# Performance work log

Hardware: AMD Instinct MI355X
Metric: run time of the kernel (lower is better)

The kernel has to match this reference:

```python
import jax, jax.numpy as jnp
import numpy as np

LN_EPS = 1e-5


def _gather(x, idx):
    # x: [B, N, C], idx: [B, N, K] -> [B, N, K, C]
    return jax.vmap(lambda xb, ib: xb[ib])(x, idx)


def setup_inputs() -> dict:
    key = jax.random.key(0)
    ks = jax.random.split(key, 8)
    B, N, K, C_in, C_out, GEO = 2, 16384, 32, 128, 128, 10
    return {
        "points": jax.random.normal(ks[0], (B, N, 3), dtype=jnp.float32),
        "features": jax.random.normal(ks[1], (B, N, C_in), dtype=jnp.float32),
        "grouped_idx": jax.random.randint(ks[2], (B, N, K), 0, N, dtype=jnp.int32),
        "w_pos": jax.random.normal(ks[3], (GEO, C_in), dtype=jnp.float32) * (GEO ** -0.5),
        "b_pos": jnp.zeros((C_in,), jnp.float32),
        "w_gcm": jax.random.normal(ks[4], (C_in, C_in), dtype=jnp.float32) * (C_in ** -0.5),
        "b_gcm": jnp.zeros((C_in,), jnp.float32),
        "w_out": jax.random.normal(ks[5], (C_in, C_out), dtype=jnp.float32) * (C_in ** -0.5),
        "b_out": jnp.zeros((C_out,), jnp.float32),
        "ln_g": jnp.ones((C_out,), jnp.float32),
        "ln_b": jnp.zeros((C_out,), jnp.float32),
    }


def reference(points, features, grouped_idx, w_pos, b_pos, w_gcm, b_gcm,
              w_out, b_out, ln_g, ln_b):
    # gather neighbor coords and features: [B, N, K, *]
    grouped_pts = _gather(points, grouped_idx)
    xyz = points[..., 0:3]                      # [B, N, 3]
    grouped_xyz = grouped_pts[..., 0:3]         # [B, N, K, 3]
    center = xyz[:, :, None, :]                 # [B, N, 1, 3]
    diff = grouped_xyz - center                 # xi - xj
    dist = jnp.linalg.norm(diff, axis=-1, keepdims=True)  # ||xi - xj||
    K = grouped_xyz.shape[2]
    geo = jnp.concatenate(
        [jnp.broadcast_to(center, grouped_xyz.shape), grouped_xyz, diff, dist],
        axis=-1)                                # [B, N, K, 10]
    expanded_f = geo @ w_pos + b_pos            # pos_proj -> [B, N, K, C_in]
    grouped_f = _gather(features, grouped_idx)  # [B, N, K, C_in]
    h = jax.nn.relu((grouped_f + expanded_f) @ w_gcm + b_gcm)  # gcm_layer
    pooled = jnp.max(h, axis=2)                 # maxpooling over neighbors
    res = pooled + features                     # residual
    o = res @ w_out + b_out                     # out Linear
    mu = jnp.mean(o, axis=-1, keepdims=True)
    var = jnp.mean((o - mu) ** 2, axis=-1, keepdims=True)
    o = (o - mu) * jax.lax.rsqrt(var + LN_EPS) * ln_g + ln_b  # LayerNorm
    return jax.nn.relu(o)
```

## Files before the change

kernel.cpp:

```cpp
#include <hip/hip_runtime.h>
#include <hip/hip_bf16.h>
#include <math.h>

typedef __attribute__((ext_vector_type(8))) short short8;
typedef __attribute__((ext_vector_type(4))) float float4v;
typedef unsigned short ushort_t;

constexpr int NPTS = 32768;
constexpr int NN   = 16384;
constexpr int KK   = 32;
constexpr int CC   = 128;
constexpr int GRP  = 16;
constexpr int SR   = 132;
#define LN_EPS 1e-5f

constexpr size_t WS_PG = 0;
constexpr size_t WS_BE = 5120;
constexpr size_t WS_WP = 8192;
constexpr size_t WS_WO = 40960;
constexpr size_t WS_FW = 73728;

__device__ __forceinline__ short f2bs(float x) {
    return (short)__builtin_bit_cast(unsigned short, __float2bfloat16(x));
}
__device__ __forceinline__ float bs2f(ushort_t u) {
    return __uint_as_float(((unsigned)u) << 16);
}

__global__ __launch_bounds__(128) void prep_fold(
    const float* __restrict__ w_pos, const float* __restrict__ b_pos,
    const float* __restrict__ w_gcm, const float* __restrict__ b_gcm,
    const float* __restrict__ w_out,
    float* __restrict__ wsPG, float* __restrict__ wsBeff,
    short* __restrict__ wsWp, short* __restrict__ wsWo)
{
    const int c = threadIdx.x, g = blockIdx.x;
    if (g < 10) {
        float s = 0.f;
        #pragma unroll
        for (int r = 0; r < 128; ++r) s += w_pos[g * 128 + r] * w_gcm[r * 128 + c];
        wsPG[g * 128 + c] = s;
        return;
    }
    if (g == 10) {
        float s = b_gcm[c];
        #pragma unroll
        for (int r = 0; r < 128; ++r) s += b_pos[r] * w_gcm[r * 128 + c];
        wsBeff[c] = s;
        return;
    }
    if (g == 11) {
        #pragma unroll 4
        for (int e = c; e < 16 * 128 * 8; e += 128) {
            const int j = e & 7, n = (e >> 3) & 127, kg = e >> 10;
            wsWp[e] = f2bs(w_gcm[(kg * 8 + j) * 128 + n]);
        }
        return;
    }
    #pragma unroll 4
    for (int e = c; e < 16 * 128 * 8; e += 128) {
        const int j = e & 7, n = (e >> 3) & 127, kg = e >> 10;
        wsWo[e] = f2bs(w_out[(kg * 8 + j) * 128 + n]);
    }
}

__global__ __launch_bounds__(256) void fw_gemm(
    const float* __restrict__ F, const short* __restrict__ wsWp,
    ushort_t* __restrict__ fwbf)
{
    const int t = threadIdx.x, wv = t >> 6;
    const int quad = (t >> 4) & 3, m = t & 15;
    const int rg = wv >> 1, ch = wv & 1;
    const int r0 = blockIdx.x * 32 + rg * 16;

    short8 bW[4][4];
    #pragma unroll
    for (int ks = 0; ks < 4; ++ks)
        #pragma unroll
        for (int n = 0; n < 4; ++n)
            bW[ks][n] = ((const short8*)wsWp)[(ks * 4 + quad) * 128 + ch * 64 + n * 16 + m];

    const float* fr = F + (size_t)(r0 + m) * CC;
    short8 A[4];
    #pragma unroll
    for (int ks = 0; ks < 4; ++ks) {
        const float4 x = *(const float4*)(fr + ks * 32 + quad * 8);
        const float4 y = *(const float4*)(fr + ks * 32 + quad * 8 + 4);
        short8 v;
        v[0]=f2bs(x.x); v[1]=f2bs(x.y); v[2]=f2bs(x.z); v[3]=f2bs(x.w);
        v[4]=f2bs(y.x); v[5]=f2bs(y.y); v[6]=f2bs(y.z); v[7]=f2bs(y.w);
        A[ks] = v;
    }

    float4v acc[4] = {};
    #pragma unroll
    for (int ks = 0; ks < 4; ++ks)
        #pragma unroll
        for (int n = 0; n < 4; ++n)
            acc[n] = __builtin_amdgcn_mfma_f32_16x16x32_bf16(A[ks], bW[ks][n], acc[n], 0, 0, 0);

    #pragma unroll
    for (int n = 0; n < 4; ++n)
        #pragma unroll
        for (int r = 0; r < 4; ++r)
            fwbf[(size_t)(r0 + quad * 4 + r) * CC + ch * 64 + n * 16 + m] =
                (ushort_t)(unsigned short)f2bs(acc[n][r]);
}

__global__ __launch_bounds__(256) void bridge_gather(
    const float* __restrict__ points, const float* __restrict__ features,
    const int*   __restrict__ gidx,
    const float* __restrict__ wsPG, const float* __restrict__ wsBeff,
    const ushort_t* __restrict__ fwbf, const short* __restrict__ wsWo,
    const float* __restrict__ b_out, const float* __restrict__ ln_g,
    const float* __restrict__ ln_b,
    float* __restrict__ out)
{
    __shared__ float4 sND[GRP * KK];
    __shared__ int    sOff[GRP * KK];
    __shared__ float4 sCen[GRP];
    __shared__ short  sRes[GRP * SR];

    float* sPS = (float*)&sND[0];
    float* sPQ = sPS + 4 * GRP;

    const int t = threadIdx.x, wv = t >> 6;
    const int quad = (t >> 4) & 3, m = t & 15;
    const int sub = t >> 7, c = t & 127;
    const int g0 = blockIdx.x * GRP;
    const int nbase = (g0 >= NN) ? NN : 0;

    #pragma unroll
    for (int e = t; e < GRP * KK; e += 256) {
        const int p = e >> 5;
        const int kn = gidx[(size_t)(g0 + p) * KK + (e & 31)];
        const int row = nbase + kn;
        const float nx = points[(size_t)row * 3 + 0];
        const float ny = points[(size_t)row * 3 + 1];
        const float nz = points[(size_t)row * 3 + 2];
        const float cx = points[(size_t)(g0 + p) * 3 + 0];
        const float cy = points[(size_t)(g0 + p) * 3 + 1];
        const float cz = points[(size_t)(g0 + p) * 3 + 2];
        const float dx = nx - cx, dy = ny - cy, dz = nz - cz;
        sND[e] = make_float4(nx, ny, nz, sqrtf(dx * dx + dy * dy + dz * dz));
        sOff[e] = row << 8;
    }
    if (t < GRP) {
        sCen[t] = make_float4(points[(size_t)(g0 + t) * 3 + 0],
                              points[(size_t)(g0 + t) * 3 + 1],
                              points[(size_t)(g0 + t) * 3 + 2], 0.f);
    }

    float pg[10];
    #pragma unroll
    for (int g = 0; g < 10; ++g) pg[g] = wsPG[g * 128 + c];
    const float pga0 = pg[0] - pg[6], pga1 = pg[1] - pg[7], pga2 = pg[2] - pg[8];
    const float pgb0 = pg[3] + pg[6], pgb1 = pg[4] + pg[7], pgb2 = pg[5] + pg[8];
    const float pgd  = pg[9];
    const float be   = wsBeff[c];

    __syncthreads();

    const char* fwc = (const char*)fwbf + c * 2;
    for (int i = 0; i < GRP / 2; ++i) {
        const int p = sub * (GRP / 2) + i;
        const float4* nd = sND + p * KK;
        const int*    of = sOff + p * KK;
        float acc = -INFINITY;
        #pragma unroll 8
        for (int k = 0; k < KK; ++k) {
            const float4 g = nd[k];
            const float fw = bs2f(*(const ushort_t*)(fwc + of[k]));
            float v = fw + g.w * pgd;
            v = fmaf(g.x, pgb0, v);
            v = fmaf(g.y, pgb1, v);
            v = fmaf(g.z, pgb2, v);
            acc = fmaxf(acc, v);
        }
        const float4 cen = sCen[p];
        const float base = fmaf(cen.x, pga0, fmaf(cen.y, pga1, fmaf(cen.z, pga2, be)));
        const float pooled = fmaxf(acc + base, 0.f);
        const float res = pooled + features[(size_t)(g0 + p) * CC + c];
        sRes[p * SR + c] = f2bs(res);
    }
    __syncthreads();

    const int col0 = wv * 32 + m;
    short8 bWo[4][2];
    #pragma unroll
    for (int ks = 0; ks < 4; ++ks)
        #pragma unroll
        for (int ntl = 0; ntl < 2; ++ntl)
            bWo[ks][ntl] = ((const short8*)wsWo)[(ks * 4 + quad) * 128 + col0 + ntl * 16];

    const short* rm = sRes + m * SR;
    float4v acc2[2] = {};
    #pragma unroll
    for (int ks = 0; ks < 4; ++ks) {
        const short8 a = *(const short8*)(rm + ks * 32 + quad * 8);
        acc2[0] = __builtin_amdgcn_mfma_f32_16x16x32_bf16(a, bWo[ks][0], acc2[0], 0, 0, 0);
        acc2[1] = __builtin_amdgcn_mfma_f32_16x16x32_bf16(a, bWo[ks][1], acc2[1], 0, 0, 0);
    }

    const float boutv[2] = { b_out[col0], b_out[col0 + 16] };
    const float lngv[2]  = { ln_g[col0], ln_g[col0 + 16] };
    const float lnbv[2]  = { ln_b[col0], ln_b[col0 + 16] };

    #pragma unroll
    for (int r = 0; r < 4; ++r) {
        const float o0 = acc2[0][r] + boutv[0];
        const float o1 = acc2[1][r] + boutv[1];
        float ss = o0 + o1, qq = o0 * o0 + o1 * o1;
        #pragma unroll
        for (int d = 1; d < 16; d <<= 1) { ss += __shfl_xor(ss, d); qq += __shfl_xor(qq, d); }
        if (m == 0) { sPS[wv * GRP + quad * 4 + r] = ss; sPQ[wv * GRP + quad * 4 + r] = qq; }
    }
    __syncthreads();

    #pragma unroll
    for (int r = 0; r < 4; ++r) {
        const int R = quad * 4 + r;
        const float S = sPS[0 * GRP + R] + sPS[1 * GRP + R] + sPS[2 * GRP + R] + sPS[3 * GRP + R];
        const float Q = sPQ[0 * GRP + R] + sPQ[1 * GRP + R] + sPQ[2 * GRP + R] + sPQ[3 * GRP + R];
        const float mu  = S * (1.f / 128.f);
        const float var = fmaxf(Q * (1.f / 128.f) - mu * mu, 0.f);
        const float rstd = rsqrtf(var + LN_EPS);
        const float o0 = acc2[0][r] + boutv[0];
        const float o1 = acc2[1][r] + boutv[1];
        const size_t base = (size_t)(g0 + R) * CC;
        out[base + col0]      = fmaxf((o0 - mu) * rstd * lngv[0] + lnbv[0], 0.f);
        out[base + col0 + 16] = fmaxf((o1 - mu) * rstd * lngv[1] + lnbv[1], 0.f);
    }
}

extern "C" void kernel_launch(void* const* d_in, const int* in_sizes, int n_in,
                              void* d_out, int out_size, void* d_ws, size_t ws_size,
                              hipStream_t stream) {
    const float* points   = (const float*)d_in[0];
    const float* features = (const float*)d_in[1];
    const int*   gidx     = (const int*)  d_in[2];
    const float* w_pos    = (const float*)d_in[3];
    const float* b_pos    = (const float*)d_in[4];
    const float* w_gcm    = (const float*)d_in[5];
    const float* b_gcm    = (const float*)d_in[6];
    const float* w_out    = (const float*)d_in[7];
    const float* b_out    = (const float*)d_in[8];
    const float* ln_g     = (const float*)d_in[9];
    const float* ln_b     = (const float*)d_in[10];
    float* out = (float*)d_out;

    char* ws = (char*)d_ws;
    float*    wsPG   = (float*)(ws + WS_PG);
    float*    wsBeff = (float*)(ws + WS_BE);
    short*    wsWp   = (short*)(ws + WS_WP);
    short*    wsWo   = (short*)(ws + WS_WO);
    ushort_t* fwbf   = (ushort_t*)(ws + WS_FW);

    hipLaunchKernelGGL(prep_fold, dim3(13), dim3(128), 0, stream,
                       w_pos, b_pos, w_gcm, b_gcm, w_out, wsPG, wsBeff, wsWp, wsWo);
    hipLaunchKernelGGL(fw_gemm, dim3(NPTS / 32), dim3(256), 0, stream,
                       features, wsWp, fwbf);
    hipLaunchKernelGGL(bridge_gather, dim3(NPTS / GRP), dim3(256), 0, stream,
                       points, features, gidx, wsPG, wsBeff, fwbf, wsWo,
                       b_out, ln_g, ln_b, out);
}
```

Before: 163.2 us.

## Fold neighbor-coordinate projection into per-point GEMM output, slim gather LDS records

```diff
diff --git a/kernel.cpp b/kernel.cpp
--- a/kernel.cpp
+++ b/kernel.cpp
@@ -65,7 +65,8 @@
 }
 
 __global__ __launch_bounds__(256) void fw_gemm(
-    const float* __restrict__ F, const short* __restrict__ wsWp,
+    const float* __restrict__ F, const float* __restrict__ points,
+    const float* __restrict__ wsPG, const short* __restrict__ wsWp,
     ushort_t* __restrict__ fwbf)
 {
     const int t = threadIdx.x, wv = t >> 6;
@@ -79,6 +80,15 @@
         #pragma unroll
         for (int n = 0; n < 4; ++n)
             bW[ks][n] = ((const short8*)wsWp)[(ks * 4 + quad) * 128 + ch * 64 + n * 16 + m];
+
+    float pgb[3][4];
+    #pragma unroll
+    for (int n = 0; n < 4; ++n) {
+        const int c = ch * 64 + n * 16 + m;
+        pgb[0][n] = wsPG[3 * 128 + c] + wsPG[6 * 128 + c];
+        pgb[1][n] = wsPG[4 * 128 + c] + wsPG[7 * 128 + c];
+        pgb[2][n] = wsPG[5 * 128 + c] + wsPG[8 * 128 + c];
+    }
 
     const float* fr = F + (size_t)(r0 + m) * CC;
     short8 A[4];
@@ -100,11 +110,17 @@
             acc[n] = __builtin_amdgcn_mfma_f32_16x16x32_bf16(A[ks], bW[ks][n], acc[n], 0, 0, 0);
 
     #pragma unroll
-    for (int n = 0; n < 4; ++n)
-        #pragma unroll
-        for (int r = 0; r < 4; ++r)
-            fwbf[(size_t)(r0 + quad * 4 + r) * CC + ch * 64 + n * 16 + m] =
-                (ushort_t)(unsigned short)f2bs(acc[n][r]);
+    for (int r = 0; r < 4; ++r) {
+        const int row = r0 + quad * 4 + r;
+        const float px = points[(size_t)row * 3 + 0];
+        const float py = points[(size_t)row * 3 + 1];
+        const float pz = points[(size_t)row * 3 + 2];
+        #pragma unroll
+        for (int n = 0; n < 4; ++n) {
+            const float v = acc[n][r] + px * pgb[0][n] + py * pgb[1][n] + pz * pgb[2][n];
+            fwbf[(size_t)row * CC + ch * 64 + n * 16 + m] = (ushort_t)(unsigned short)f2bs(v);
+        }
+    }
 }
 
 __global__ __launch_bounds__(256) void bridge_gather(
@@ -116,12 +132,11 @@
     const float* __restrict__ ln_b,
     float* __restrict__ out)
 {
-    __shared__ float4 sND[GRP * KK];
-    __shared__ int    sOff[GRP * KK];
+    __shared__ int2   sOD[GRP * KK];
     __shared__ float4 sCen[GRP];
     __shared__ short  sRes[GRP * SR];
 
-    float* sPS = (float*)&sND[0];
+    float* sPS = (float*)&sOD[0];
     float* sPQ = sPS + 4 * GRP;
 
     const int t = threadIdx.x, wv = t >> 6;
@@ -135,15 +150,11 @@
         const int p = e >> 5;
         const int kn = gidx[(size_t)(g0 + p) * KK + (e & 31)];
         const int row = nbase + kn;
-        const float nx = points[(size_t)row * 3 + 0];
-        const float ny = points[(size_t)row * 3 + 1];
-        const float nz = points[(size_t)row * 3 + 2];
-        const float cx = points[(size_t)(g0 + p) * 3 + 0];
-        const float cy = points[(size_t)(g0 + p) * 3 + 1];
-        const float cz = points[(size_t)(g0 + p) * 3 + 2];
-        const float dx = nx - cx, dy = ny - cy, dz = nz - cz;
-        sND[e] = make_float4(nx, ny, nz, sqrtf(dx * dx + dy * dy + dz * dz));
-        sOff[e] = row << 8;
+        const float dx = points[(size_t)row * 3 + 0] - points[(size_t)(g0 + p) * 3 + 0];
+        const float dy = points[(size_t)row * 3 + 1] - points[(size_t)(g0 + p) * 3 + 1];
+        const float dz = points[(size_t)row * 3 + 2] - points[(size_t)(g0 + p) * 3 + 2];
+        const float dist = sqrtf(dx * dx + dy * dy + dz * dz);
+        sOD[e] = make_int2(row << 7, __float_as_int(dist));
     }
     if (t < GRP) {
         sCen[t] = make_float4(points[(size_t)(g0 + t) * 3 + 0],
@@ -151,31 +162,23 @@
                               points[(size_t)(g0 + t) * 3 + 2], 0.f);
     }
 
-    float pg[10];
-    #pragma unroll
-    for (int g = 0; g < 10; ++g) pg[g] = wsPG[g * 128 + c];
-    const float pga0 = pg[0] - pg[6], pga1 = pg[1] - pg[7], pga2 = pg[2] - pg[8];
-    const float pgb0 = pg[3] + pg[6], pgb1 = pg[4] + pg[7], pgb2 = pg[5] + pg[8];
-    const float pgd  = pg[9];
+    const float pga0 = wsPG[0 * 128 + c] - wsPG[6 * 128 + c];
+    const float pga1 = wsPG[1 * 128 + c] - wsPG[7 * 128 + c];
+    const float pga2 = wsPG[2 * 128 + c] - wsPG[8 * 128 + c];
+    const float pgd  = wsPG[9 * 128 + c];
     const float be   = wsBeff[c];
 
     __syncthreads();
 
-    const char* fwc = (const char*)fwbf + c * 2;
     for (int i = 0; i < GRP / 2; ++i) {
         const int p = sub * (GRP / 2) + i;
-        const float4* nd = sND + p * KK;
-        const int*    of = sOff + p * KK;
+        const int2* od = sOD + p * KK;
         float acc = -INFINITY;
-        #pragma unroll 8
+        #pragma unroll 16
         for (int k = 0; k < KK; ++k) {
-            const float4 g = nd[k];
-            const float fw = bs2f(*(const ushort_t*)(fwc + of[k]));
-            float v = fw + g.w * pgd;
-            v = fmaf(g.x, pgb0, v);
-            v = fmaf(g.y, pgb1, v);
-            v = fmaf(g.z, pgb2, v);
-            acc = fmaxf(acc, v);
+            const int2 e = od[k];
+            const float fw = bs2f(fwbf[(unsigned)(e.x | c)]);
+            acc = fmaxf(acc, fmaf(__int_as_float(e.y), pgd, fw));
         }
         const float4 cen = sCen[p];
         const float base = fmaf(cen.x, pga0, fmaf(cen.y, pga1, fmaf(cen.z, pga2, be)));
@@ -259,7 +262,7 @@
     hipLaunchKernelGGL(prep_fold, dim3(13), dim3(128), 0, stream,
                        w_pos, b_pos, w_gcm, b_gcm, w_out, wsPG, wsBeff, wsWp, wsWo);
     hipLaunchKernelGGL(fw_gemm, dim3(NPTS / 32), dim3(256), 0, stream,
-                       features, wsWp, fwbf);
+                       features, points, wsPG, wsWp, fwbf);
     hipLaunchKernelGGL(bridge_gather, dim3(NPTS / GRP), dim3(256), 0, stream,
                        points, features, gidx, wsPG, wsBeff, fwbf, wsWo,
                        b_out, ln_g, ln_b, out);
```

Measured after the change: 208.3 us. +27.7%, slower.
